# Kernel optimization log

Hardware: AMD Instinct MI355X
Metric: run time of the kernel (lower is better)

## Reference

```python
import jax, jax.numpy as jnp
import numpy as np

N_QUBITS = 24

def setup_inputs() -> dict:
    key = jax.random.key(0)
    k1, k2, k3 = jax.random.split(key, 3)
    n = 1 << N_QUBITS
    state_re = jax.random.normal(k1, (n,), dtype=jnp.float32)
    state_im = jax.random.normal(k2, (n,), dtype=jnp.float32)
    theta = jax.random.uniform(k3, (1,), dtype=jnp.float32)
    return {"state_re": state_re, "state_im": state_im, "theta": theta}

def reference(state_re, state_im, theta):
    # Rx(theta) = [[cos(t/2), -i sin(t/2)], [-i sin(t/2), cos(t/2)]]
    t2 = theta[0] * 0.5
    c = jnp.cos(t2).astype(jnp.complex64)
    s = (-1j * jnp.sin(t2)).astype(jnp.complex64)
    M = jnp.stack([jnp.stack([c, s]), jnp.stack([s, c])])  # [2,2]
    psi = (state_re + 1j * state_im).astype(jnp.complex64)
    # target qubit 0 -> bit index n_qubits-1 (most significant bit of state index)
    psi2 = psi.reshape(2, -1)                # [2, 2^(n-1)]
    out = jnp.einsum('ij,jk->ik', M, psi2).reshape(-1)
    # return as stacked real/imag float32 [2, 2^n]
    return jnp.stack([out.real, out.imag]).astype(jnp.float32)
```

## Files before the change

### kernel.cpp

```cpp
#include <hip/hip_runtime.h>


typedef float f32x4 __attribute__((ext_vector_type(4)));

constexpr int NV = 1 << 21;
constexpr int S  = 1 << 20;

__device__ __forceinline__ void rx_math(
    float c, float s,
    const f32x4& a_re, const f32x4& a_im,
    const f32x4& b_re, const f32x4& b_im,
    f32x4& o0_re, f32x4& o0_im, f32x4& o1_re, f32x4& o1_im)
{
    o0_re = c * a_re + s * b_im;
    o0_im = c * a_im - s * b_re;
    o1_re = c * b_re + s * a_im;
    o1_im = c * b_im - s * a_re;
}

__global__ __launch_bounds__(256) void rx_gate_kernel(
    const f32x4* __restrict__ sre,
    const f32x4* __restrict__ sim,
    const float* __restrict__ theta,
    f32x4* __restrict__ out)
{
    const int t = blockIdx.x * blockDim.x + threadIdx.x;
    const int j0 = t;
    const int j1 = t + S;

    const float t2 = theta[0] * 0.5f;
    const float s = sinf(t2);
    const float c = cosf(t2);

    const f32x4 a0_re = sre[j0];
    const f32x4 a0_im = sim[j0];
    const f32x4 b0_re = sre[j0 + NV];
    const f32x4 b0_im = sim[j0 + NV];
    const f32x4 a1_re = sre[j1];
    const f32x4 a1_im = sim[j1];
    const f32x4 b1_re = sre[j1 + NV];
    const f32x4 b1_im = sim[j1 + NV];

    f32x4 o0_re, o0_im, o1_re, o1_im;
    rx_math(c, s, a0_re, a0_im, b0_re, b0_im, o0_re, o0_im, o1_re, o1_im);

    __builtin_nontemporal_store(o0_re, &out[j0]);
    __builtin_nontemporal_store(o1_re, &out[j0 + NV]);
    __builtin_nontemporal_store(o0_im, &out[j0 + 2 * NV]);
    __builtin_nontemporal_store(o1_im, &out[j0 + 3 * NV]);

    rx_math(c, s, a1_re, a1_im, b1_re, b1_im, o0_re, o0_im, o1_re, o1_im);

    __builtin_nontemporal_store(o0_re, &out[j1]);
    __builtin_nontemporal_store(o1_re, &out[j1 + NV]);
    __builtin_nontemporal_store(o0_im, &out[j1 + 2 * NV]);
    __builtin_nontemporal_store(o1_im, &out[j1 + 3 * NV]);
}

extern "C" void kernel_launch(void* const* d_in, const int* in_sizes, int n_in,
                              void* d_out, int out_size, void* d_ws, size_t ws_size,
                              hipStream_t stream) {
    const f32x4* sre   = (const f32x4*)d_in[0];
    const f32x4* sim   = (const f32x4*)d_in[1];
    const float* theta = (const float*)d_in[2];
    f32x4* out = (f32x4*)d_out;

    const int threads = 256;
    const int blocks  = S / threads;
    rx_gate_kernel<<<blocks, threads, 0, stream>>>(sre, sim, theta, out);
}
```

Measured before the change: 256.4 us.

## Split Rx gate work into independent re/im half-pairs per block

Each block now handles one of two decoupled halves of the computation. Even blocks read a_re and b_im and write o0_re and o1_im; odd blocks read a_im and b_re and write o0_im and o1_re. Each thread does one float4 pair instead of two full quartets, which lowers per-thread register and load pressure and quadruples the thread count. Nontemporal stores are also replaced with plain stores, which may change cache behaviour for the output writes.

```diff
diff --git a/kernel.cpp b/kernel.cpp
--- a/kernel.cpp
+++ b/kernel.cpp
@@ -4,19 +4,6 @@
 typedef float f32x4 __attribute__((ext_vector_type(4)));
 
 constexpr int NV = 1 << 21;
-constexpr int S  = 1 << 20;
-
-__device__ __forceinline__ void rx_math(
-    float c, float s,
-    const f32x4& a_re, const f32x4& a_im,
-    const f32x4& b_re, const f32x4& b_im,
-    f32x4& o0_re, f32x4& o0_im, f32x4& o1_re, f32x4& o1_im)
-{
-    o0_re = c * a_re + s * b_im;
-    o0_im = c * a_im - s * b_re;
-    o1_re = c * b_re + s * a_im;
-    o1_im = c * b_im - s * a_re;
-}
 
 __global__ __launch_bounds__(256) void rx_gate_kernel(
     const f32x4* __restrict__ sre,
@@ -24,37 +11,28 @@
     const float* __restrict__ theta,
     f32x4* __restrict__ out)
 {
-    const int t = blockIdx.x * blockDim.x + threadIdx.x;
-    const int j0 = t;
-    const int j1 = t + S;
-
     const float t2 = theta[0] * 0.5f;
     const float s = sinf(t2);
     const float c = cosf(t2);
 
-    const f32x4 a0_re = sre[j0];
-    const f32x4 a0_im = sim[j0];
-    const f32x4 b0_re = sre[j0 + NV];
-    const f32x4 b0_im = sim[j0 + NV];
-    const f32x4 a1_re = sre[j1];
-    const f32x4 a1_im = sim[j1];
-    const f32x4 b1_re = sre[j1 + NV];
-    const f32x4 b1_im = sim[j1 + NV];
+    const int bid = blockIdx.x;
+    const int i   = (bid >> 1) * blockDim.x + threadIdx.x;
 
-    f32x4 o0_re, o0_im, o1_re, o1_im;
-    rx_math(c, s, a0_re, a0_im, b0_re, b0_im, o0_re, o0_im, o1_re, o1_im);
-
-    __builtin_nontemporal_store(o0_re, &out[j0]);
-    __builtin_nontemporal_store(o1_re, &out[j0 + NV]);
-    __builtin_nontemporal_store(o0_im, &out[j0 + 2 * NV]);
-    __builtin_nontemporal_store(o1_im, &out[j0 + 3 * NV]);
-
-    rx_math(c, s, a1_re, a1_im, b1_re, b1_im, o0_re, o0_im, o1_re, o1_im);
-
-    __builtin_nontemporal_store(o0_re, &out[j1]);
-    __builtin_nontemporal_store(o1_re, &out[j1 + NV]);
-    __builtin_nontemporal_store(o0_im, &out[j1 + 2 * NV]);
-    __builtin_nontemporal_store(o1_im, &out[j1 + 3 * NV]);
+    if ((bid & 1) == 0) {
+        const f32x4 a_re = sre[i];
+        const f32x4 b_im = sim[i + NV];
+        const f32x4 o0_re = c * a_re + s * b_im;
+        const f32x4 o1_im = c * b_im - s * a_re;
+        out[i]          = o0_re;
+        out[i + 3 * NV] = o1_im;
+    } else {
+        const f32x4 a_im = sim[i];
+        const f32x4 b_re = sre[i + NV];
+        const f32x4 o0_im = c * a_im - s * b_re;
+        const f32x4 o1_re = c * b_re + s * a_im;
+        out[i + 2 * NV] = o0_im;
+        out[i + NV]     = o1_re;
+    }
 }
 
 extern "C" void kernel_launch(void* const* d_in, const int* in_sizes, int n_in,
@@ -66,6 +44,6 @@
     f32x4* out = (f32x4*)d_out;
 
     const int threads = 256;
-    const int blocks  = S / threads;
+    const int blocks  = 2 * (NV / threads);
     rx_gate_kernel<<<blocks, threads, 0, stream>>>(sre, sim, theta, out);
 }
```

Result: faster. 235.4 us (-8.2%).
